# Optimization experiments

Measured on AMD Instinct MI355X. Metric: run time of the kernel, lower is better.

## Reference

```python
import jax, jax.numpy as jnp
import numpy as np

N, E, D, C, M = 50000, 600000, 128, 40, 25000


def setup_inputs() -> dict:
    key = jax.random.key(0)
    ks = jax.random.split(key, 10)
    s = 1.0 / np.sqrt(D)
    return {
        "x": jax.random.normal(ks[0], (N, D), jnp.float32),
        "edge_index": jax.random.randint(ks[1], (2, E), 0, N, jnp.int64),
        "node_label_index": jax.random.randint(ks[2], (M,), 0, N, jnp.int64),
        "W0": jax.random.normal(ks[3], (D, D), jnp.float32) * s,
        "b0": jnp.zeros((D,), jnp.float32),
        "W1": jax.random.normal(ks[4], (D, D), jnp.float32) * s,
        "b1": jnp.zeros((D,), jnp.float32),
        "W2": jax.random.normal(ks[5], (D, D), jnp.float32) * s,
        "b2": jnp.zeros((D,), jnp.float32),
        "W3": jax.random.normal(ks[6], (D, D), jnp.float32) * s,
        "b3": jnp.zeros((D,), jnp.float32),
        "Wh": jax.random.normal(ks[7], (D, C), jnp.float32) * s,
        "bh": jnp.zeros((C,), jnp.float32),
    }


def _gcn(x, W, b, src, dst, dinv):
    h = x @ W                                    # [N, D']
    norm = (dinv[src] * dinv[dst])[:, None]      # [E, 1]
    agg = jax.ops.segment_sum(h[src] * norm, dst, num_segments=x.shape[0])
    return agg + h * (dinv ** 2)[:, None] + b    # self-loop term + bias


def reference(x, edge_index, node_label_index, W0, b0, W1, b1, W2, b2, W3, b3, Wh, bh):
    src, dst = edge_index[0], edge_index[1]
    # degree with self-loops (PyG counts in-degree on dst after add_self_loops)
    deg = 1.0 + jax.ops.segment_sum(jnp.ones((src.shape[0],), x.dtype), dst,
                                    num_segments=x.shape[0])
    dinv = jax.lax.rsqrt(deg)

    cell0 = _gcn(x, W0, b0, src, dst, dinv)
    cell1 = _gcn(jax.nn.relu(cell0), W1, b1, src, dst, dinv)
    cell2 = (_gcn(jax.nn.relu(cell0), W2, b2, src, dst, dinv)
             + _gcn(jax.nn.relu(cell1), W2, b2, src, dst, dinv))
    cell3 = (_gcn(jax.nn.relu(cell0), W3, b3, src, dst, dinv)
             + _gcn(jax.nn.relu(cell1), W3, b3, src, dst, dinv)
             + _gcn(jax.nn.relu(cell2), W3, b3, src, dst, dinv))

    feat = jax.nn.log_softmax(cell3, axis=1)
    pred = (feat @ Wh + bh)[node_label_index]    # [M, C]
    return pred
```

## Files before the change

### kernel.cpp

```cpp
#include <hip/hip_runtime.h>
#include <hip/hip_bf16.h>
#include <cstdint>
#include <cstddef>

#define DIM 128

typedef __attribute__((ext_vector_type(8))) short bf16x8;
typedef __attribute__((ext_vector_type(4))) float f32x4;

__device__ __forceinline__ unsigned short f2bf(float f) {
    __hip_bfloat16 h = __float2bfloat16(f);
    return *(unsigned short*)&h;
}
__device__ __forceinline__ unsigned pack_bf2(float a, float b) {
    return (unsigned)f2bf(a) | ((unsigned)f2bf(b) << 16);
}
__device__ __forceinline__ float bflo(unsigned u) { return __uint_as_float(u << 16); }
__device__ __forceinline__ float bfhi(unsigned u) { return __uint_as_float(u & 0xffff0000u); }

union U4B8 { uint4 q; bf16x8 v; };

__global__ __launch_bounds__(256)
void k_init(const int* __restrict__ dst, int* __restrict__ count,
            int* __restrict__ rank, int e, int egrid,
            const float* __restrict__ W0, const float* __restrict__ W1,
            const float* __restrict__ W2, const float* __restrict__ W3,
            const float* __restrict__ Wh, const float* __restrict__ b3,
            const float* __restrict__ bh,
            unsigned short* __restrict__ Wpk,
            unsigned short* __restrict__ WcombP,
            float* __restrict__ whs, float* __restrict__ bcomb,
            unsigned short* __restrict__ H, unsigned short* __restrict__ H2,
            unsigned short* __restrict__ Abuf,
            float* __restrict__ dinv, int n, int C) {
    if ((int)blockIdx.x < egrid) {
        int i = blockIdx.x * 256 + threadIdx.x;
        if (i < e) rank[i] = atomicAdd(&count[dst[i]], 1);
        return;
    }
    const int NW = 4 * DIM * DIM;
    const int NH = 3 * 4 * 64 * 8;
    int g = (blockIdx.x - egrid) * 256 + threadIdx.x;
    if (g < NW) {
        int j   = g & 7;
        int ln  = (g >> 3) & 63;
        int kc  = (g >> 9) & 3;
        int nt  = (g >> 11) & 7;
        int mat = g >> 14;
        const float* W = (mat == 0) ? W0 : (mat == 1) ? W1 : (mat == 2) ? W2 : W3;
        int k = kc * 32 + (ln >> 4) * 8 + j;
        int nc = nt * 16 + (ln & 15);
        Wpk[g] = f2bf(W[k * DIM + nc]);
    } else if (g < NW + NH) {
        int gg = g - NW;
        int j  = gg & 7;
        int ln = (gg >> 3) & 63;
        int kc = (gg >> 9) & 3;
        int nt = gg >> 11;
        int k  = kc * 32 + (ln >> 4) * 8 + j;
        int nc = nt * 16 + (ln & 15);
        float s = 0.f;
        if (nc < C) {
            for (int d = 0; d < DIM; ++d) s += W3[k * DIM + d] * Wh[d * C + nc];
        }
        WcombP[gg] = f2bf(s);
    } else if (g < NW + NH + 64) {
        int c = g - NW - NH;
        if (c < C) {
            float s = 0.f, t = 0.f;
            for (int d = 0; d < DIM; ++d) {
                float w = Wh[d * C + c];
                s += w;
                t += b3[d] * w;
            }
            whs[c]   = s;
            bcomb[c] = 3.0f * t + bh[c];
        }
    } else if (g < NW + NH + 64 + 16) {
        int t = g - (NW + NH + 64);
        uint4 z; z.x = z.y = z.z = z.w = 0u;
        ((uint4*)H)[(size_t)n * 16 + t] = z;
    } else if (g < NW + NH + 64 + 32) {
        int t = g - (NW + NH + 64 + 16);
        uint4 z; z.x = z.y = z.z = z.w = 0u;
        ((uint4*)H2)[(size_t)n * 16 + t] = z;
    } else if (g < NW + NH + 64 + 48) {
        int t = g - (NW + NH + 64 + 32);
        uint4 z; z.x = z.y = z.z = z.w = 0u;
        ((uint4*)Abuf)[(size_t)n * 16 + t] = z;
    } else if (g == NW + NH + 64 + 48) {
        dinv[n] = 0.f;
    }
}

__global__ __launch_bounds__(1024)
void k_scanA(const int* __restrict__ count, int* __restrict__ partial,
             int* __restrict__ bsum, float* __restrict__ dinv, int n) {
    __shared__ int wsum[16];
    int tid = threadIdx.x, lane = tid & 63, wid = tid >> 6;
    int i = blockIdx.x * 1024 + tid;
    int v = (i < n) ? count[i] : 0;
    if (i < n) dinv[i] = rsqrtf(1.0f + (float)v);
    int x = v;
    #pragma unroll
    for (int off = 1; off < 64; off <<= 1) {
        int y = __shfl_up(x, off, 64);
        if (lane >= off) x += y;
    }
    if (lane == 63) wsum[wid] = x;
    __syncthreads();
    int waveoff = 0, total = 0;
    #pragma unroll
    for (int w = 0; w < 16; ++w) {
        int s = wsum[w];
        if (w < wid) waveoff += s;
        total += s;
    }
    if (i < n) partial[i] = x + waveoff;
    if (tid == 0) bsum[blockIdx.x] = total;
}

__global__ __launch_bounds__(1024)
void k_scanB(const int* __restrict__ partial, const int* __restrict__ bsum,
             int* __restrict__ row_ptr, int n, int nb) {
    __shared__ int s_off;
    int tid = threadIdx.x;
    if (tid < 64) {
        int carry = 0;
        for (int base = 0; base < nb; base += 64) {
            int idx = base + tid;
            int v = (idx < nb && idx < blockIdx.x) ? bsum[idx] : 0;
            #pragma unroll
            for (int off = 32; off > 0; off >>= 1) v += __shfl_xor(v, off, 64);
            carry += v;
        }
        if (tid == 0) s_off = carry;
    }
    __syncthreads();
    int off = s_off;
    int i = blockIdx.x * 1024 + tid;
    if (i < n) row_ptr[i + 1] = partial[i] + off;
    if (blockIdx.x == 0 && tid == 0) row_ptr[0] = 0;
}

__global__ __launch_bounds__(256)
void k_fillmm(const float* __restrict__ in, const unsigned short* __restrict__ Wpk,
              const float* __restrict__ dinv, unsigned short* __restrict__ outp, int n,
              const int* __restrict__ src, const int* __restrict__ dst,
              const int* __restrict__ rank, const int* __restrict__ row_ptr,
              int* __restrict__ colv, int e, int mmg) {
    if ((int)blockIdx.x >= mmg) {
        int i = (blockIdx.x - mmg) * 256 + threadIdx.x;
        if (i < e) {
            int d = dst[i];
            int r = rank[i];
            colv[row_ptr[d] + r] = src[i];
        }
        return;
    }
    int wv   = threadIdx.x >> 6;
    int lane = threadIdx.x & 63;
    int r0   = blockIdx.x * 64 + wv * 16;
    int m    = lane & 15;
    int quad = lane >> 4;

    bf16x8 afr[4];
    int arow = r0 + m;
    bool rowok = arow < n;
    const float* ap = in + (size_t)arow * DIM + quad * 8;
    #pragma unroll
    for (int kc = 0; kc < 4; ++kc) {
        float4 p0, p1;
        if (rowok) {
            p0 = *(const float4*)(ap + kc * 32);
            p1 = *(const float4*)(ap + kc * 32 + 4);
        } else {
            p0.x = p0.y = p0.z = p0.w = 0.f;
            p1.x = p1.y = p1.z = p1.w = 0.f;
        }
        union { bf16x8 v; unsigned short u[8]; } a;
        a.u[0] = f2bf(p0.x); a.u[1] = f2bf(p0.y);
        a.u[2] = f2bf(p0.z); a.u[3] = f2bf(p0.w);
        a.u[4] = f2bf(p1.x); a.u[5] = f2bf(p1.y);
        a.u[6] = f2bf(p1.z); a.u[7] = f2bf(p1.w);
        afr[kc] = a.v;
    }

    float dsc[4];
    #pragma unroll
    for (int t = 0; t < 4; ++t) {
        int r = r0 + quad * 4 + t;
        dsc[t] = (r < n) ? dinv[r] : 0.f;
    }

    const uint4* wp = (const uint4*)Wpk;
    #pragma unroll
    for (int nt = 0; nt < 8; ++nt) {
        f32x4 acc = {0.f, 0.f, 0.f, 0.f};
        #pragma unroll
        for (int kc = 0; kc < 4; ++kc) {
            U4B8 b; b.q = wp[(nt * 4 + kc) * 64 + lane];
            acc = __builtin_amdgcn_mfma_f32_16x16x32_bf16(afr[kc], b.v, acc, 0, 0, 0);
        }
        int colb = nt * 16 + m;
        #pragma unroll
        for (int t = 0; t < 4; ++t) {
            int r = r0 + quad * 4 + t;
            if (r < n)
                outp[(size_t)r * DIM + colb] = f2bf(dsc[t] * acc[t]);
        }
    }
}

__global__ __launch_bounds__(1024)
void k_prop_mm(const unsigned short* __restrict__ h, const int* __restrict__ row_ptr,
               const int* __restrict__ col, const float* __restrict__ dinv,
               const float* __restrict__ bias, float bscale,
               const unsigned short* addin, unsigned short* __restrict__ outp,
               const unsigned short* __restrict__ Wnext,
               unsigned short* __restrict__ outH, int n) {
    __shared__ uint4 Vs[16 * 17];
    __shared__ float Ds[16];
    int wid  = threadIdx.x >> 6;
    int lane = threadIdx.x & 63;
    int node = blockIdx.x * 16 + wid;
    bool valid = node < n;
    int gnode = valid ? node : 0;
    int beg = 0, end = 0;
    if (valid) { beg = row_ptr[gnode]; end = row_ptr[gnode + 1]; }
    float di = dinv[gnode];
    int qid = lane >> 4, fo = lane & 15;
    const uint4* h16 = (const uint4*)h;
    uint4 sd = h16[((unsigned)gnode << 4) | fo];
    float aL0 = 0.f, aH0 = 0.f, aL1 = 0.f, aH1 = 0.f;
    float aL2 = 0.f, aH2 = 0.f, aL3 = 0.f, aH3 = 0.f;
    float bL0 = 0.f, bH0 = 0.f, bL1 = 0.f, bH1 = 0.f;
    float bL2 = 0.f, bH2 = 0.f, bL3 = 0.f, bH3 = 0.f;
    int j = beg + qid;
    int s0 = (j < end) ? col[j] : n;
    int s1 = (j + 4 < end) ? col[j + 4] : n;
    while (s0 != n) {
        uint4 d0 = h16[((unsigned)s0 << 4) | fo];
        uint4 d1 = h16[((unsigned)s1 << 4) | fo];
        int jn = j + 8;
        s0 = (jn < end) ? col[jn] : n;
        s1 = (jn + 4 < end) ? col[jn + 4] : n;
        j = jn;
        aL0 += bflo(d0.x); aH0 += bfhi(d0.x);
        aL1 += bflo(d0.y); aH1 += bfhi(d0.y);
        aL2 += bflo(d0.z); aH2 += bfhi(d0.z);
        aL3 += bflo(d0.w); aH3 += bfhi(d0.w);
        bL0 += bflo(d1.x); bH0 += bfhi(d1.x);
        bL1 += bflo(d1.y); bH1 += bfhi(d1.y);
        bL2 += bflo(d1.z); bH2 += bfhi(d1.z);
        bL3 += bflo(d1.w); bH3 += bfhi(d1.w);
    }
    uint4 av; av.x = av.y = av.z = av.w = 0u;
    if (addin) av = ((const uint4*)addin)[(size_t)gnode * 16 + fo];
    aL0 += bL0; aH0 += bH0; aL1 += bL1; aH1 += bH1;
    aL2 += bL2; aH2 += bH2; aL3 += bL3; aH3 += bH3;
    aL0 += __shfl_xor(aL0, 16, 64); aL0 += __shfl_xor(aL0, 32, 64);
    aH0 += __shfl_xor(aH0, 16, 64); aH0 += __shfl_xor(aH0, 32, 64);
    aL1 += __shfl_xor(aL1, 16, 64); aL1 += __shfl_xor(aL1, 32, 64);
    aH1 += __shfl_xor(aH1, 16, 64); aH1 += __shfl_xor(aH1, 32, 64);
    aL2 += __shfl_xor(aL2, 16, 64); aL2 += __shfl_xor(aL2, 32, 64);
    aH2 += __shfl_xor(aH2, 16, 64); aH2 += __shfl_xor(aH2, 32, 64);
    aL3 += __shfl_xor(aL3, 16, 64); aL3 += __shfl_xor(aL3, 32, 64);
    aH3 += __shfl_xor(aH3, 16, 64); aH3 += __shfl_xor(aH3, 32, 64);
    aL0 += bflo(sd.x); aH0 += bfhi(sd.x);
    aL1 += bflo(sd.y); aH1 += bfhi(sd.y);
    aL2 += bflo(sd.z); aH2 += bfhi(sd.z);
    aL3 += bflo(sd.w); aH3 += bfhi(sd.w);
    if (lane < 16) {
        const float4* b4 = (const float4*)bias;
        float4 bA = b4[2 * fo], bB = b4[2 * fo + 1];
        float r0x = fmaxf(fmaf(bscale, bA.x, di * aL0), 0.f);
        float r0y = fmaxf(fmaf(bscale, bA.y, di * aH0), 0.f);
        float r0z = fmaxf(fmaf(bscale, bA.z, di * aL1), 0.f);
        float r0w = fmaxf(fmaf(bscale, bA.w, di * aH1), 0.f);
        float r1x = fmaxf(fmaf(bscale, bB.x, di * aL2), 0.f);
        float r1y = fmaxf(fmaf(bscale, bB.y, di * aH2), 0.f);
        float r1z = fmaxf(fmaf(bscale, bB.z, di * aL3), 0.f);
        float r1w = fmaxf(fmaf(bscale, bB.w, di * aH3), 0.f);
        r0x += bflo(av.x); r0y += bfhi(av.x);
        r0z += bflo(av.y); r0w += bfhi(av.y);
        r1x += bflo(av.z); r1y += bfhi(av.z);
        r1z += bflo(av.w); r1w += bfhi(av.w);
        uint4 o;
        o.x = pack_bf2(r0x, r0y);
        o.y = pack_bf2(r0z, r0w);
        o.z = pack_bf2(r1x, r1y);
        o.w = pack_bf2(r1z, r1w);
        Vs[wid * 17 + fo] = o;
        if (valid)
            ((uint4*)outp)[(size_t)gnode * 16 + fo] = o;
        if (fo == 0) Ds[wid] = di;
    }
    __syncthreads();

    if (wid < 8) {
        int nt = wid;
        int mm = lane & 15, quad = lane >> 4;
        bf16x8 afr[4];
        #pragma unroll
        for (int kc = 0; kc < 4; ++kc) {
            U4B8 a; a.q = Vs[mm * 17 + kc * 4 + quad];
            afr[kc] = a.v;
        }
        f32x4 acc = {0.f, 0.f, 0.f, 0.f};
        const uint4* wp = (const uint4*)Wnext;
        #pragma unroll
        for (int kc = 0; kc < 4; ++kc) {
            U4B8 b; b.q = wp[(nt * 4 + kc) * 64 + lane];
            acc = __builtin_amdgcn_mfma_f32_16x16x32_bf16(afr[kc], b.v, acc, 0, 0, 0);
        }
        int colb = nt * 16 + mm;
        #pragma unroll
        for (int t = 0; t < 4; ++t) {
            int row = quad * 4 + t;
            int r = blockIdx.x * 16 + row;
            if (r < n)
                outH[(size_t)r * DIM + colb] = f2bf(Ds[row] * acc[t]);
        }
    }
}

__global__ __launch_bounds__(256)
void k_prop(const unsigned short* __restrict__ h, const int* __restrict__ row_ptr,
            const int* __restrict__ col, const float* __restrict__ dinv,
            const float* __restrict__ bias, float bscale,
            const unsigned short* addin, unsigned short* __restrict__ outp, int n) {
    int node = (blockIdx.x * 256 + threadIdx.x) >> 6;
    int lane = threadIdx.x & 63;
    if (node >= n) return;
    int beg = row_ptr[node], end = row_ptr[node + 1];
    float di = dinv[node];
    int qid = lane >> 4;
    int fo  = lane & 15;
    const uint4* h16 = (const uint4*)h;
    uint4 sd = h16[((unsigned)node << 4) | fo];
    float aL0 = 0.f, aH0 = 0.f, aL1 = 0.f, aH1 = 0.f;
    float aL2 = 0.f, aH2 = 0.f, aL3 = 0.f, aH3 = 0.f;
    float bL0 = 0.f, bH0 = 0.f, bL1 = 0.f, bH1 = 0.f;
    float bL2 = 0.f, bH2 = 0.f, bL3 = 0.f, bH3 = 0.f;
    int j = beg + qid;
    int s0 = (j < end) ? col[j] : n;
    int s1 = (j + 4 < end) ? col[j + 4] : n;
    while (s0 != n) {
        uint4 d0 = h16[((unsigned)s0 << 4) | fo];
        uint4 d1 = h16[((unsigned)s1 << 4) | fo];
        int jn = j + 8;
        s0 = (jn < end) ? col[jn] : n;
        s1 = (jn + 4 < end) ? col[jn + 4] : n;
        j = jn;
        aL0 += bflo(d0.x); aH0 += bfhi(d0.x);
        aL1 += bflo(d0.y); aH1 += bfhi(d0.y);
        aL2 += bflo(d0.z); aH2 += bfhi(d0.z);
        aL3 += bflo(d0.w); aH3 += bfhi(d0.w);
        bL0 += bflo(d1.x); bH0 += bfhi(d1.x);
        bL1 += bflo(d1.y); bH1 += bfhi(d1.y);
        bL2 += bflo(d1.z); bH2 += bfhi(d1.z);
        bL3 += bflo(d1.w); bH3 += bfhi(d1.w);
    }
    uint4 av; av.x = av.y = av.z = av.w = 0u;
    if (addin) av = ((const uint4*)addin)[(size_t)node * 16 + fo];
    aL0 += bL0; aH0 += bH0; aL1 += bL1; aH1 += bH1;
    aL2 += bL2; aH2 += bH2; aL3 += bL3; aH3 += bH3;
    aL0 += __shfl_xor(aL0, 16, 64); aL0 += __shfl_xor(aL0, 32, 64);
    aH0 += __shfl_xor(aH0, 16, 64); aH0 += __shfl_xor(aH0, 32, 64);
    aL1 += __shfl_xor(aL1, 16, 64); aL1 += __shfl_xor(aL1, 32, 64);
    aH1 += __shfl_xor(aH1, 16, 64); aH1 += __shfl_xor(aH1, 32, 64);
    aL2 += __shfl_xor(aL2, 16, 64); aL2 += __shfl_xor(aL2, 32, 64);
    aH2 += __shfl_xor(aH2, 16, 64); aH2 += __shfl_xor(aH2, 32, 64);
    aL3 += __shfl_xor(aL3, 16, 64); aL3 += __shfl_xor(aL3, 32, 64);
    aH3 += __shfl_xor(aH3, 16, 64); aH3 += __shfl_xor(aH3, 32, 64);
    aL0 += bflo(sd.x); aH0 += bfhi(sd.x);
    aL1 += bflo(sd.y); aH1 += bfhi(sd.y);
    aL2 += bflo(sd.z); aH2 += bfhi(sd.z);
    aL3 += bflo(sd.w); aH3 += bfhi(sd.w);
    if (lane < 16) {
        const float4* b4 = (const float4*)bias;
        float4 bA = b4[2 * fo], bB = b4[2 * fo + 1];
        float r0x = fmaxf(fmaf(bscale, bA.x, di * aL0), 0.f);
        float r0y = fmaxf(fmaf(bscale, bA.y, di * aH0), 0.f);
        float r0z = fmaxf(fmaf(bscale, bA.z, di * aL1), 0.f);
        float r0w = fmaxf(fmaf(bscale, bA.w, di * aH1), 0.f);
        float r1x = fmaxf(fmaf(bscale, bB.x, di * aL2), 0.f);
        float r1y = fmaxf(fmaf(bscale, bB.y, di * aH2), 0.f);
        float r1z = fmaxf(fmaf(bscale, bB.z, di * aL3), 0.f);
        float r1w = fmaxf(fmaf(bscale, bB.w, di * aH3), 0.f);
        r0x += bflo(av.x); r0y += bfhi(av.x);
        r0z += bflo(av.y); r0w += bfhi(av.y);
        r1x += bflo(av.z); r1y += bfhi(av.z);
        r1z += bflo(av.w); r1w += bfhi(av.w);
        size_t base = (size_t)node * 16 + fo;
        uint4 o;
        o.x = pack_bf2(r0x, r0y);
        o.y = pack_bf2(r0z, r0w);
        o.z = pack_bf2(r1x, r1y);
        o.w = pack_bf2(r1z, r1w);
        ((uint4*)outp)[base] = o;
    }
}

__global__ __launch_bounds__(1024)
void k_propv_fused(const unsigned short* __restrict__ A, const int* __restrict__ row_ptr,
                   const int* __restrict__ col, const float* __restrict__ dinv,
                   const float* __restrict__ b3, float bscale,
                   const int* __restrict__ labels,
                   const unsigned short* __restrict__ W3pk,
                   const unsigned short* __restrict__ WcombP,
                   const float* __restrict__ whs, const float* __restrict__ bcomb,
                   float* __restrict__ outp, int m_total, int C, int n) {
    __shared__ uint4 Vs[16 * 17];
    __shared__ float Ds[16];
    __shared__ float Mred[8 * 16];
    __shared__ float Sred[8 * 16];
    __shared__ float Ls[16];
    int wid  = threadIdx.x >> 6;
    int lane = threadIdx.x & 63;
    int m = blockIdx.x * 16 + wid;
    bool valid = m < m_total;
    int node = valid ? labels[m] : 0;
    int beg = 0, end = 0;
    if (valid) { beg = row_ptr[node]; end = row_ptr[node + 1]; }
    float di = dinv[node];
    int qid = lane >> 4, fo = lane & 15;
    const uint4* h16 = (const uint4*)A;
    uint4 sd = h16[((unsigned)node << 4) | fo];
    float aL0 = 0.f, aH0 = 0.f, aL1 = 0.f, aH1 = 0.f;
    float aL2 = 0.f, aH2 = 0.f, aL3 = 0.f, aH3 = 0.f;
    float bL0 = 0.f, bH0 = 0.f, bL1 = 0.f, bH1 = 0.f;
    float bL2 = 0.f, bH2 = 0.f, bL3 = 0.f, bH3 = 0.f;
    int j = beg + qid;
    int s0 = (j < end) ? col[j] : n;
    int s1 = (j + 4 < end) ? col[j + 4] : n;
    float w0 = dinv[s0], w1 = dinv[s1];
    while (s0 != n) {
        uint4 d0 = h16[((unsigned)s0 << 4) | fo];
        uint4 d1 = h16[((unsigned)s1 << 4) | fo];
        float cw0 = w0, cw1 = w1;
        int jn = j + 8;
        s0 = (jn < end) ? col[jn] : n;
        s1 = (jn + 4 < end) ? col[jn + 4] : n;
        w0 = dinv[s0]; w1 = dinv[s1];
        j = jn;
        aL0 = fmaf(cw0, bflo(d0.x), aL0); aH0 = fmaf(cw0, bfhi(d0.x), aH0);
        aL1 = fmaf(cw0, bflo(d0.y), aL1); aH1 = fmaf(cw0, bfhi(d0.y), aH1);
        aL2 = fmaf(cw0, bflo(d0.z), aL2); aH2 = fmaf(cw0, bfhi(d0.z), aH2);
        aL3 = fmaf(cw0, bflo(d0.w), aL3); aH3 = fmaf(cw0, bfhi(d0.w), aH3);
        bL0 = fmaf(cw1, bflo(d1.x), bL0); bH0 = fmaf(cw1, bfhi(d1.x), bH0);
        bL1 = fmaf(cw1, bflo(d1.y), bL1); bH1 = fmaf(cw1, bfhi(d1.y), bH1);
        bL2 = fmaf(cw1, bflo(d1.z), bL2); bH2 = fmaf(cw1, bfhi(d1.z), bH2);
        bL3 = fmaf(cw1, bflo(d1.w), bL3); bH3 = fmaf(cw1, bfhi(d1.w), bH3);
    }
    aL0 += bL0; aH0 += bH0; aL1 += bL1; aH1 += bH1;
    aL2 += bL2; aH2 += bH2; aL3 += bL3; aH3 += bH3;
    aL0 += __shfl_xor(aL0, 16, 64); aL0 += __shfl_xor(aL0, 32, 64);
    aH0 += __shfl_xor(aH0, 16, 64); aH0 += __shfl_xor(aH0, 32, 64);
    aL1 += __shfl_xor(aL1, 16, 64); aL1 += __shfl_xor(aL1, 32, 64);
    aH1 += __shfl_xor(aH1, 16, 64); aH1 += __shfl_xor(aH1, 32, 64);
    aL2 += __shfl_xor(aL2, 16, 64); aL2 += __shfl_xor(aL2, 32, 64);
    aH2 += __shfl_xor(aH2, 16, 64); aH2 += __shfl_xor(aH2, 32, 64);
    aL3 += __shfl_xor(aL3, 16, 64); aL3 += __shfl_xor(aL3, 32, 64);
    aH3 += __shfl_xor(aH3, 16, 64); aH3 += __shfl_xor(aH3, 32, 64);
    aL0 = fmaf(di, bflo(sd.x), aL0); aH0 = fmaf(di, bfhi(sd.x), aH0);
    aL1 = fmaf(di, bflo(sd.y), aL1); aH1 = fmaf(di, bfhi(sd.y), aH1);
    aL2 = fmaf(di, bflo(sd.z), aL2); aH2 = fmaf(di, bfhi(sd.z), aH2);
    aL3 = fmaf(di, bflo(sd.w), aL3); aH3 = fmaf(di, bfhi(sd.w), aH3);
    if (lane < 16) {
        uint4 o;
        o.x = pack_bf2(aL0, aH0);
        o.y = pack_bf2(aL1, aH1);
        o.z = pack_bf2(aL2, aH2);
        o.w = pack_bf2(aL3, aH3);
        Vs[wid * 17 + fo] = o;
    }
    if (lane == 0) Ds[wid] = di;
    __syncthreads();

    f32x4 hacc = {0.f, 0.f, 0.f, 0.f};
    float cell[4] = {0.f, 0.f, 0.f, 0.f};
    float gmx[4]  = {0.f, 0.f, 0.f, 0.f};
    int mm = lane & 15, quad = lane >> 4;
    if (wid < 8) {
        int nt = wid;
        bf16x8 afr[4];
        #pragma unroll
        for (int kc = 0; kc < 4; ++kc) {
            U4B8 a; a.q = Vs[mm * 17 + kc * 4 + quad];
            afr[kc] = a.v;
        }
        f32x4 acc = {0.f, 0.f, 0.f, 0.f};
        const uint4* wp = (const uint4*)W3pk;
        #pragma unroll
        for (int kc = 0; kc < 4; ++kc) {
            U4B8 b; b.q = wp[(nt * 4 + kc) * 64 + lane];
            acc = __builtin_amdgcn_mfma_f32_16x16x32_bf16(afr[kc], b.v, acc, 0, 0, 0);
        }
        float b3c = bscale * b3[nt * 16 + mm];
        #pragma unroll
        for (int t = 0; t < 4; ++t) {
            int row = quad * 4 + t;
            cell[t] = fmaf(Ds[row], acc[t], b3c);
            float mxv = cell[t];
            #pragma unroll
            for (int off = 1; off < 16; off <<= 1)
                mxv = fmaxf(mxv, __shfl_xor(mxv, off, 64));
            if (mm == 0) Mred[nt * 16 + row] = mxv;
        }
    } else if (wid < 11) {
        int nth = wid - 8;
        bf16x8 afr[4];
        #pragma unroll
        for (int kc = 0; kc < 4; ++kc) {
            U4B8 a; a.q = Vs[mm * 17 + kc * 4 + quad];
            afr[kc] = a.v;
        }
        const uint4* wp = (const uint4*)WcombP;
        #pragma unroll
        for (int kc = 0; kc < 4; ++kc) {
            U4B8 b; b.q = wp[(nth * 4 + kc) * 64 + lane];
            hacc = __builtin_amdgcn_mfma_f32_16x16x32_bf16(afr[kc], b.v, hacc, 0, 0, 0);
        }
    }
    __syncthreads();

    if (wid < 8) {
        int nt = wid;
        #pragma unroll
        for (int t = 0; t < 4; ++t) {
            int row = quad * 4 + t;
            float g = Mred[row];
            #pragma unroll
            for (int i = 1; i < 8; ++i) g = fmaxf(g, Mred[i * 16 + row]);
            gmx[t] = g;
            float e = expf(cell[t] - g);
            #pragma unroll
            for (int off = 1; off < 16; off <<= 1) e += __shfl_xor(e, off, 64);
            if (mm == 0) Sred[nt * 16 + row] = e;
        }
    }
    __syncthreads();

    if (wid == 0 && mm == 0) {
        #pragma unroll
        for (int t = 0; t < 4; ++t) {
            int row = quad * 4 + t;
            float s = Sred[row];
            #pragma unroll
            for (int i = 1; i < 8; ++i) s += Sred[i * 16 + row];
            Ls[row] = gmx[t] + logf(s);
        }
    }
    __syncthreads();

    if (wid >= 8 && wid < 11) {
        int nth = wid - 8;
        int colc = nth * 16 + mm;
        if (colc < C) {
            float wsc = whs[colc], bc = bcomb[colc];
            #pragma unroll
            for (int t = 0; t < 4; ++t) {
                int row = quad * 4 + t;
                int r = blockIdx.x * 16 + row;
                if (r < m_total)
                    outp[(size_t)r * C + colc] =
                        fmaf(Ds[row], hacc[t], bc) - Ls[row] * wsc;
            }
        }
    }
}

extern "C" void kernel_launch(void* const* d_in, const int* in_sizes, int n_in,
                              void* d_out, int out_size, void* d_ws, size_t ws_size,
                              hipStream_t stream) {
    const float* x      = (const float*)d_in[0];
    const int*   edges  = (const int*)d_in[1];
    const int*   labels = (const int*)d_in[2];
    const float* W0 = (const float*)d_in[3];
    const float* b0 = (const float*)d_in[4];
    const float* W1 = (const float*)d_in[5];
    const float* b1 = (const float*)d_in[6];
    const float* W2 = (const float*)d_in[7];
    const float* b2 = (const float*)d_in[8];
    const float* W3 = (const float*)d_in[9];
    const float* b3 = (const float*)d_in[10];
    const float* Wh = (const float*)d_in[11];
    const float* bh = (const float*)d_in[12];
    float* out = (float*)d_out;

    const int N = in_sizes[0] / DIM;
    const int E = in_sizes[1] / 2;
    const int M = in_sizes[2];
    const int C = in_sizes[12];

    char* ws = (char*)d_ws;
    auto alloc = [&](size_t bytes) {
        char* p = ws;
        ws += (bytes + 255) & ~(size_t)255;
        return p;
    };
    float* dinv    = (float*)alloc((size_t)(N + 1) * 4);
    int*   count   = (int*)  alloc((size_t)N * 4);
    int*   row_ptr = (int*)  alloc((size_t)(N + 1) * 4);
    int*   rank    = (int*)  alloc((size_t)E * 4);
    int*   partial = (int*)  alloc((size_t)N * 4);
    int*   bsum    = (int*)  alloc(64 * 4);
    int*   col     = (int*)  alloc((size_t)E * 4);
    float* whs     = (float*)alloc(256);
    float* bcomb   = (float*)alloc(256);
    unsigned short* Wpk    = (unsigned short*)alloc((size_t)4 * DIM * DIM * 2);
    unsigned short* WcombP = (unsigned short*)alloc((size_t)3 * 4 * 64 * 8 * 2);
    unsigned short* H   = (unsigned short*)alloc((size_t)(N + 1) * DIM * 2);
    unsigned short* H2  = (unsigned short*)alloc((size_t)(N + 1) * DIM * 2);
    unsigned short* R0  = (unsigned short*)alloc((size_t)N * DIM * 2);
    unsigned short* A   = (unsigned short*)alloc((size_t)(N + 1) * DIM * 2);

    const int* src = edges;
    const int* dst = edges + E;

    int egrid  = (E + 255) / 256;
    int sgrid  = (N + 1023) / 1024;
    int mmgrid = (N + 63) / 64;
    int pgrid  = (N + 3) / 4;
    int fgrid  = (N + 15) / 16;
    const int FR = DIM * DIM;
    const int NPACK = 4 * FR + 3 * 4 * 64 * 8 + 64 + 49;
    int packgrid = (NPACK + 255) / 256;

    hipMemsetAsync(count, 0, (size_t)N * 4, stream);
    k_init <<<egrid + packgrid, 256, 0, stream>>>(dst, count, rank, E, egrid,
                                                  W0, W1, W2, W3, Wh, b3, bh,
                                                  Wpk, WcombP, whs, bcomb,
                                                  H, H2, A, dinv, N, C);
    k_scanA<<<sgrid, 1024, 0, stream>>>(count, partial, bsum, dinv, N);
    k_scanB<<<sgrid, 1024, 0, stream>>>(partial, bsum, row_ptr, N, sgrid);
    k_fillmm<<<mmgrid + egrid, 256, 0, stream>>>(x, Wpk, dinv, H, N,
                                                 src, dst, rank, row_ptr, col, E, mmgrid);
    k_prop_mm<<<fgrid, 1024, 0, stream>>>(H, row_ptr, col, dinv, b0, 1.f,
                                          nullptr, R0, Wpk + 1 * FR, H2, N);
    k_prop_mm<<<fgrid, 1024, 0, stream>>>(H2, row_ptr, col, dinv, b1, 1.f,
                                          R0, A, Wpk + 2 * FR, H, N);
    k_prop    <<<pgrid, 256, 0, stream>>>(H, row_ptr, col, dinv, b2, 2.f, A, A, N);
    k_propv_fused<<<(M + 15) / 16, 1024, 0, stream>>>(A, row_ptr, col, dinv, b3, 3.f,
                                                      labels, Wpk + 3 * FR, WcombP,
                                                      whs, bcomb, out, M, C, N);
}
```

Before: 269.0 us.

## Fuse two-pass scan into single-pass decoupled scan; unroll gather loops to four

Result: slower. 278.8 us (+3.6%).

```diff
diff --git a/kernel.cpp b/kernel.cpp
--- a/kernel.cpp
+++ b/kernel.cpp
@@ -32,7 +32,7 @@
             float* __restrict__ whs, float* __restrict__ bcomb,
             unsigned short* __restrict__ H, unsigned short* __restrict__ H2,
             unsigned short* __restrict__ Abuf,
-            float* __restrict__ dinv, int n, int C) {
+            float* __restrict__ dinv, int* __restrict__ bsum, int n, int C) {
     if ((int)blockIdx.x < egrid) {
         int i = blockIdx.x * 256 + threadIdx.x;
         if (i < e) rank[i] = atomicAdd(&count[dst[i]], 1);
@@ -40,6 +40,7 @@
     }
     const int NW = 4 * DIM * DIM;
     const int NH = 3 * 4 * 64 * 8;
+    const int TB = NW + NH + 64;
     int g = (blockIdx.x - egrid) * 256 + threadIdx.x;
     if (g < NW) {
         int j   = g & 7;
@@ -76,27 +77,31 @@
             whs[c]   = s;
             bcomb[c] = 3.0f * t + bh[c];
         }
-    } else if (g < NW + NH + 64 + 16) {
-        int t = g - (NW + NH + 64);
+    } else if (g < TB + 16) {
+        int t = g - TB;
         uint4 z; z.x = z.y = z.z = z.w = 0u;
         ((uint4*)H)[(size_t)n * 16 + t] = z;
-    } else if (g < NW + NH + 64 + 32) {
-        int t = g - (NW + NH + 64 + 16);
+    } else if (g < TB + 32) {
+        int t = g - (TB + 16);
         uint4 z; z.x = z.y = z.z = z.w = 0u;
         ((uint4*)H2)[(size_t)n * 16 + t] = z;
-    } else if (g < NW + NH + 64 + 48) {
-        int t = g - (NW + NH + 64 + 32);
+    } else if (g < TB + 48) {
+        int t = g - (TB + 32);
         uint4 z; z.x = z.y = z.z = z.w = 0u;
         ((uint4*)Abuf)[(size_t)n * 16 + t] = z;
-    } else if (g == NW + NH + 64 + 48) {
+    } else if (g < TB + 112) {
+        bsum[g - (TB + 48)] = 0;
+    } else if (g == TB + 112) {
         dinv[n] = 0.f;
     }
 }
 
 __global__ __launch_bounds__(1024)
-void k_scanA(const int* __restrict__ count, int* __restrict__ partial,
-             int* __restrict__ bsum, float* __restrict__ dinv, int n) {
+void k_scan(const int* __restrict__ count, int* __restrict__ bsum,
+            int* __restrict__ row_ptr, float* __restrict__ dinv, int n, int nb) {
     __shared__ int wsum[16];
+    __shared__ int s_off;
+    const int FLAG = 1 << 30;
     int tid = threadIdx.x, lane = tid & 63, wid = tid >> 6;
     int i = blockIdx.x * 1024 + tid;
     int v = (i < n) ? count[i] : 0;
@@ -116,30 +121,25 @@
         if (w < wid) waveoff += s;
         total += s;
     }
-    if (i < n) partial[i] = x + waveoff;
-    if (tid == 0) bsum[blockIdx.x] = total;
-}
-
-__global__ __launch_bounds__(1024)
-void k_scanB(const int* __restrict__ partial, const int* __restrict__ bsum,
-             int* __restrict__ row_ptr, int n, int nb) {
-    __shared__ int s_off;
-    int tid = threadIdx.x;
+    if (tid == 0) atomicExch(&bsum[blockIdx.x], total | FLAG);
     if (tid < 64) {
         int carry = 0;
         for (int base = 0; base < nb; base += 64) {
             int idx = base + tid;
-            int v = (idx < nb && idx < blockIdx.x) ? bsum[idx] : 0;
+            int vv = 0;
+            if (idx < nb && idx < (int)blockIdx.x) {
+                do { vv = atomicAdd(&bsum[idx], 0); } while (!(vv & FLAG));
+                vv &= ~FLAG;
+            }
             #pragma unroll
-            for (int off = 32; off > 0; off >>= 1) v += __shfl_xor(v, off, 64);
-            carry += v;
+            for (int off = 32; off > 0; off >>= 1) vv += __shfl_xor(vv, off, 64);
+            carry += vv;
         }
         if (tid == 0) s_off = carry;
     }
     __syncthreads();
     int off = s_off;
-    int i = blockIdx.x * 1024 + tid;
-    if (i < n) row_ptr[i + 1] = partial[i] + off;
+    if (i < n) row_ptr[i + 1] = x + waveoff + off;
     if (blockIdx.x == 0 && tid == 0) row_ptr[0] = 0;
 }
 
@@ -237,14 +237,20 @@
     float bL0 = 0.f, bH0 = 0.f, bL1 = 0.f, bH1 = 0.f;
     float bL2 = 0.f, bH2 = 0.f, bL3 = 0.f, bH3 = 0.f;
     int j = beg + qid;
-    int s0 = (j < end) ? col[j] : n;
-    int s1 = (j + 4 < end) ? col[j + 4] : n;
+    int s0 = (j      < end) ? col[j]      : n;
+    int s1 = (j + 4  < end) ? col[j + 4]  : n;
+    int s2 = (j + 8  < end) ? col[j + 8]  : n;
+    int s3 = (j + 12 < end) ? col[j + 12] : n;
     while (s0 != n) {
         uint4 d0 = h16[((unsigned)s0 << 4) | fo];
         uint4 d1 = h16[((unsigned)s1 << 4) | fo];
-        int jn = j + 8;
-        s0 = (jn < end) ? col[jn] : n;
-        s1 = (jn + 4 < end) ? col[jn + 4] : n;
+        uint4 d2 = h16[((unsigned)s2 << 4) | fo];
+        uint4 d3 = h16[((unsigned)s3 << 4) | fo];
+        int jn = j + 16;
+        s0 = (jn      < end) ? col[jn]      : n;
+        s1 = (jn + 4  < end) ? col[jn + 4]  : n;
+        s2 = (jn + 8  < end) ? col[jn + 8]  : n;
+        s3 = (jn + 12 < end) ? col[jn + 12] : n;
         j = jn;
         aL0 += bflo(d0.x); aH0 += bfhi(d0.x);
         aL1 += bflo(d0.y); aH1 += bfhi(d0.y);
@@ -254,6 +260,14 @@
         bL1 += bflo(d1.y); bH1 += bfhi(d1.y);
         bL2 += bflo(d1.z); bH2 += bfhi(d1.z);
         bL3 += bflo(d1.w); bH3 += bfhi(d1.w);
+        aL0 += bflo(d2.x); aH0 += bfhi(d2.x);
+        aL1 += bflo(d2.y); aH1 += bfhi(d2.y);
+        aL2 += bflo(d2.z); aH2 += bfhi(d2.z);
+        aL3 += bflo(d2.w); aH3 += bfhi(d2.w);
+        bL0 += bflo(d3.x); bH0 += bfhi(d3.x);
+        bL1 += bflo(d3.y); bH1 += bfhi(d3.y);
+        bL2 += bflo(d3.z); bH2 += bfhi(d3.z);
+        bL3 += bflo(d3.w); bH3 += bfhi(d3.w);
     }
     uint4 av; av.x = av.y = av.z = av.w = 0u;
     if (addin) av = ((const uint4*)addin)[(size_t)gnode * 16 + fo];
@@ -344,14 +358,20 @@
     float bL0 = 0.f, bH0 = 0.f, bL1 = 0.f, bH1 = 0.f;
     float bL2 = 0.f, bH2 = 0.f, bL3 = 0.f, bH3 = 0.f;
     int j = beg + qid;
-    int s0 = (j < end) ? col[j] : n;
-    int s1 = (j + 4 < end) ? col[j + 4] : n;
+    int s0 = (j      < end) ? col[j]      : n;
+    int s1 = (j + 4  < end) ? col[j + 4]  : n;
+    int s2 = (j + 8  < end) ? col[j + 8]  : n;
+    int s3 = (j + 12 < end) ? col[j + 12] : n;
     while (s0 != n) {
         uint4 d0 = h16[((unsigned)s0 << 4) | fo];
         uint4 d1 = h16[((unsigned)s1 << 4) | fo];
-        int jn = j + 8;
-        s0 = (jn < end) ? col[jn] : n;
-        s1 = (jn + 4 < end) ? col[jn + 4] : n;
+        uint4 d2 = h16[((unsigned)s2 << 4) | fo];
+        uint4 d3 = h16[((unsigned)s3 << 4) | fo];
+        int jn = j + 16;
+        s0 = (jn      < end) ? col[jn]      : n;
+        s1 = (jn + 4  < end) ? col[jn + 4]  : n;
+        s2 = (jn + 8  < end) ? col[jn + 8]  : n;
+        s3 = (jn + 12 < end) ? col[jn + 12] : n;
         j = jn;
         aL0 += bflo(d0.x); aH0 += bfhi(d0.x);
         aL1 += bflo(d0.y); aH1 += bfhi(d0.y);
@@ -361,6 +381,14 @@
         bL1 += bflo(d1.y); bH1 += bfhi(d1.y);
         bL2 += bflo(d1.z); bH2 += bfhi(d1.z);
         bL3 += bflo(d1.w); bH3 += bfhi(d1.w);
+        aL0 += bflo(d2.x); aH0 += bfhi(d2.x);
+        aL1 += bflo(d2.y); aH1 += bfhi(d2.y);
+        aL2 += bflo(d2.z); aH2 += bfhi(d2.z);
+        aL3 += bflo(d2.w); aH3 += bfhi(d2.w);
+        bL0 += bflo(d3.x); bH0 += bfhi(d3.x);
+        bL1 += bflo(d3.y); bH1 += bfhi(d3.y);
+        bL2 += bflo(d3.z); bH2 += bfhi(d3.z);
+        bL3 += bflo(d3.w); bH3 += bfhi(d3.w);
     }
     uint4 av; av.x = av.y = av.z = av.w = 0u;
     if (addin) av = ((const uint4*)addin)[(size_t)node * 16 + fo];
@@ -433,17 +461,23 @@
     float bL0 = 0.f, bH0 = 0.f, bL1 = 0.f, bH1 = 0.f;
     float bL2 = 0.f, bH2 = 0.f, bL3 = 0.f, bH3 = 0.f;
     int j = beg + qid;
-    int s0 = (j < end) ? col[j] : n;
-    int s1 = (j + 4 < end) ? col[j + 4] : n;
-    float w0 = dinv[s0], w1 = dinv[s1];
+    int s0 = (j      < end) ? col[j]      : n;
+    int s1 = (j + 4  < end) ? col[j + 4]  : n;
+    int s2 = (j + 8  < end) ? col[j + 8]  : n;
+    int s3 = (j + 12 < end) ? col[j + 12] : n;
+    float w0 = dinv[s0], w1 = dinv[s1], w2 = dinv[s2], w3 = dinv[s3];
     while (s0 != n) {
         uint4 d0 = h16[((unsigned)s0 << 4) | fo];
         uint4 d1 = h16[((unsigned)s1 << 4) | fo];
-        float cw0 = w0, cw1 = w1;
-        int jn = j + 8;
-        s0 = (jn < end) ? col[jn] : n;
-        s1 = (jn + 4 < end) ? col[jn + 4] : n;
-        w0 = dinv[s0]; w1 = dinv[s1];
+        uint4 d2 = h16[((unsigned)s2 << 4) | fo];
+        uint4 d3 = h16[((unsigned)s3 << 4) | fo];
+        float cw0 = w0, cw1 = w1, cw2 = w2, cw3 = w3;
+        int jn = j + 16;
+        s0 = (jn      < end) ? col[jn]      : n;
+        s1 = (jn + 4  < end) ? col[jn + 4]  : n;
+        s2 = (jn + 8  < end) ? col[jn + 8]  : n;
+        s3 = (jn + 12 < end) ? col[jn + 12] : n;
+        w0 = dinv[s0]; w1 = dinv[s1]; w2 = dinv[s2]; w3 = dinv[s3];
         j = jn;
         aL0 = fmaf(cw0, bflo(d0.x), aL0); aH0 = fmaf(cw0, bfhi(d0.x), aH0);
         aL1 = fmaf(cw0, bflo(d0.y), aL1); aH1 = fmaf(cw0, bfhi(d0.y), aH1);
@@ -453,6 +487,14 @@
         bL1 = fmaf(cw1, bflo(d1.y), bL1); bH1 = fmaf(cw1, bfhi(d1.y), bH1);
         bL2 = fmaf(cw1, bflo(d1.z), bL2); bH2 = fmaf(cw1, bfhi(d1.z), bH2);
         bL3 = fmaf(cw1, bflo(d1.w), bL3); bH3 = fmaf(cw1, bfhi(d1.w), bH3);
+        aL0 = fmaf(cw2, bflo(d2.x), aL0); aH0 = fmaf(cw2, bfhi(d2.x), aH0);
+        aL1 = fmaf(cw2, bflo(d2.y), aL1); aH1 = fmaf(cw2, bfhi(d2.y), aH1);
+        aL2 = fmaf(cw2, bflo(d2.z), aL2); aH2 = fmaf(cw2, bfhi(d2.z), aH2);
+        aL3 = fmaf(cw2, bflo(d2.w), aL3); aH3 = fmaf(cw2, bfhi(d2.w), aH3);
+        bL0 = fmaf(cw3, bflo(d3.x), bL0); bH0 = fmaf(cw3, bfhi(d3.x), bH0);
+        bL1 = fmaf(cw3, bflo(d3.y), bL1); bH1 = fmaf(cw3, bfhi(d3.y), bH1);
+        bL2 = fmaf(cw3, bflo(d3.z), bL2); bH2 = fmaf(cw3, bfhi(d3.z), bH2);
+        bL3 = fmaf(cw3, bflo(d3.w), bL3); bH3 = fmaf(cw3, bfhi(d3.w), bH3);
     }
     aL0 += bL0; aH0 += bH0; aL1 += bL1; aH1 += bH1;
     aL2 += bL2; aH2 += bH2; aL3 += bL3; aH3 += bH3;
@@ -605,7 +647,6 @@
     int*   count   = (int*)  alloc((size_t)N * 4);
     int*   row_ptr = (int*)  alloc((size_t)(N + 1) * 4);
     int*   rank    = (int*)  alloc((size_t)E * 4);
-    int*   partial = (int*)  alloc((size_t)N * 4);
     int*   bsum    = (int*)  alloc(64 * 4);
     int*   col     = (int*)  alloc((size_t)E * 4);
     float* whs     = (float*)alloc(256);
@@ -626,16 +667,15 @@
     int pgrid  = (N + 3) / 4;
     int fgrid  = (N + 15) / 16;
     const int FR = DIM * DIM;
-    const int NPACK = 4 * FR + 3 * 4 * 64 * 8 + 64 + 49;
+    const int NPACK = 4 * FR + 3 * 4 * 64 * 8 + 64 + 113;
     int packgrid = (NPACK + 255) / 256;
 
     hipMemsetAsync(count, 0, (size_t)N * 4, stream);
     k_init <<<egrid + packgrid, 256, 0, stream>>>(dst, count, rank, E, egrid,
                                                   W0, W1, W2, W3, Wh, b3, bh,
                                                   Wpk, WcombP, whs, bcomb,
-                                                  H, H2, A, dinv, N, C);
-    k_scanA<<<sgrid, 1024, 0, stream>>>(count, partial, bsum, dinv, N);
-    k_scanB<<<sgrid, 1024, 0, stream>>>(partial, bsum, row_ptr, N, sgrid);
+                                                  H, H2, A, dinv, bsum, N, C);
+    k_scan <<<sgrid, 1024, 0, stream>>>(count, bsum, row_ptr, dinv, N, sgrid);
     k_fillmm<<<mmgrid + egrid, 256, 0, stream>>>(x, Wpk, dinv, H, N,
                                                  src, dst, rank, row_ptr, col, E, mmgrid);
     k_prop_mm<<<fgrid, 1024, 0, stream>>>(H, row_ptr, col, dinv, b0, 1.f,
```
